# Kernel optimization log

Hardware: AMD Instinct MI355X
Metric: run time of the kernel (lower is better)

Reference implementation:

```python
import jax, jax.numpy as jnp
import numpy as np

B, S, D, H, E = 4, 1024, 1024, 16, 4
HD = D // H
FF = 4 * D
EPS = 1e-5


def _ln(x):
    # normalize only; per-expert affine applied by caller
    mu = jnp.mean(x, axis=-1, keepdims=True)
    var = jnp.mean(jnp.square(x - mu), axis=-1, keepdims=True)
    return (x - mu) * jax.lax.rsqrt(var + EPS)


def setup_inputs() -> dict:
    key = jax.random.key(0)
    ks = jax.random.split(key, 12)
    s = 0.02
    inp = {
        "x": jax.random.normal(ks[0], (B, S, D), jnp.float32),
        # attention router
        "Wr_a": jax.random.normal(ks[1], (D, E), jnp.float32) * s,
        "br_a": jnp.zeros((E,), jnp.float32),
        # per-expert attention params
        "g_a": jnp.ones((E, D), jnp.float32),
        "b_a": jnp.zeros((E, D), jnp.float32),
        "Wqkv": jax.random.normal(ks[2], (E, D, 3 * D), jnp.float32) * s,
        "bqkv": jnp.zeros((E, 3 * D), jnp.float32),
        "Wpr": jax.random.normal(ks[3], (E, D, D), jnp.float32) * s,
        "bpr": jnp.zeros((E, D), jnp.float32),
        # MLP router
        "Wr_m": jax.random.normal(ks[4], (D, E), jnp.float32) * s,
        "br_m": jnp.zeros((E,), jnp.float32),
        # per-expert MLP params
        "g_m": jnp.ones((E, D), jnp.float32),
        "b_m": jnp.zeros((E, D), jnp.float32),
        "Wfc": jax.random.normal(ks[5], (E, D, FF), jnp.float32) * s,
        "bfc": jnp.zeros((E, FF), jnp.float32),
        "Wp2": jax.random.normal(ks[6], (E, FF, D), jnp.float32) * s,
        "bp2": jnp.zeros((E, D), jnp.float32),
    }
    return inp


def _block(x, Wr_a, br_a, g_a, b_a, Wqkv, bqkv, Wpr, bpr,
           Wr_m, br_m, g_m, b_m, Wfc, bfc, Wp2, bp2):
    N = B * S
    h = x.reshape(N, D)

    # ---- MoT attention (routing_all_possible_path: dense score-weighted mix) ----
    score = jax.nn.softmax(h @ Wr_a + br_a, axis=-1)          # [N,E]
    hn = _ln(h)                                                # shared normalization
    hln = hn[None, :, :] * g_a[:, None, :] + b_a[:, None, :]  # [E,N,D]
    qkv_e = jnp.einsum('end,edf->enf', hln, Wqkv) + bqkv[:, None, :]  # [E,N,3D]
    qkv = jnp.einsum('ne,enf->nf', score, qkv_e)               # [N,3D]

    q, k, v = jnp.split(qkv.reshape(B, S, 3 * D), 3, axis=-1)
    q = q.reshape(B, S, H, HD).transpose(0, 2, 1, 3)           # [B,H,S,hd]
    k = k.reshape(B, S, H, HD).transpose(0, 2, 1, 3)
    v = v.reshape(B, S, H, HD).transpose(0, 2, 1, 3)

    aw = jnp.einsum('bhqd,bhkd->bhqk', q, k) / jnp.sqrt(jnp.float32(HD))
    causal = jnp.tril(jnp.ones((S, S), bool))
    aw = jnp.where(causal, aw, jnp.finfo(aw.dtype).min)
    p = jax.nn.softmax(aw, axis=-1)
    a = jnp.einsum('bhqk,bhkd->bhqd', p, v)                    # [B,H,S,hd]
    a = a.transpose(0, 2, 1, 3).reshape(N, D)

    attn_out = jnp.einsum('ne,nd,edf->nf', score, a, Wpr) + score @ bpr
    y = x + attn_out.reshape(B, S, D)

    # ---- MoT MLP (same dense routed-expert pattern) ----
    h2 = y.reshape(N, D)
    score2 = jax.nn.softmax(h2 @ Wr_m + br_m, axis=-1)         # [N,E]
    hn2 = _ln(h2)
    hln2 = hn2[None, :, :] * g_m[:, None, :] + b_m[:, None, :]  # [E,N,D]
    inter = jax.nn.gelu(jnp.einsum('end,edf->enf', hln2, Wfc) + bfc[:, None, :])  # [E,N,FF]
    mlp_out = jnp.einsum('ne,enf,efd->nd', score2, inter, Wp2) + score2 @ bp2
    return y + mlp_out.reshape(B, S, D)


def reference(x, Wr_a, br_a, g_a, b_a, Wqkv, bqkv, Wpr, bpr,
              Wr_m, br_m, g_m, b_m, Wfc, bfc, Wp2, bp2):
    return _block(x, Wr_a, br_a, g_a, b_a, Wqkv, bqkv, Wpr, bpr,
                  Wr_m, br_m, g_m, b_m, Wfc, bfc, Wp2, bp2)
```

## Files before the change

### kernel.cpp

```cpp
#include <hip/hip_runtime.h>
#include <hip/hip_bf16.h>

typedef __bf16 bf16x8 __attribute__((ext_vector_type(8)));
typedef float f32x4 __attribute__((ext_vector_type(4)));
typedef unsigned short u16;
typedef u16 u16x8 __attribute__((ext_vector_type(8)));
typedef u16 u16x4 __attribute__((ext_vector_type(4)));

#define B_ 4
#define S_ 1024
#define D_ 1024
#define E_ 4
#define H_ 16
#define FF_ 4096
#define N_ 4096

__device__ __forceinline__ u16 f2bf(float f) {
  __hip_bfloat16 h = __float2bfloat16(f);
  return *reinterpret_cast<u16*>(&h);
}
__device__ __forceinline__ float bf2f(u16 v) {
  return __uint_as_float(((unsigned)v) << 16);
}

#define BAR()                         \
  {                                   \
    asm volatile("" ::: "memory");    \
    __builtin_amdgcn_s_barrier();     \
    asm volatile("" ::: "memory");    \
  }

__global__ __launch_bounds__(256) void tcvt(const float* __restrict__ src,
                                            u16* __restrict__ dst, int R, int C) {
  __shared__ float t[32][33];
  int r0 = blockIdx.y * 32, c0 = blockIdx.x * 32;
  int tx = threadIdx.x, ty = threadIdx.y;
#pragma unroll
  for (int i = 0; i < 4; i++)
    t[ty + i * 8][tx] = src[(long)(r0 + ty + i * 8) * C + c0 + tx];
  __syncthreads();
#pragma unroll
  for (int i = 0; i < 4; i++)
    dst[(long)(c0 + ty + i * 8) * R + r0 + tx] = f2bf(t[tx][ty + i * 8]);
}

template <int YMODE>
__global__ __launch_bounds__(256) void ln_router_expand(
    const float* __restrict__ X, const float* __restrict__ Wr, const float* __restrict__ br,
    const float* __restrict__ g, const float* __restrict__ bb,
    float* __restrict__ score_out, u16* __restrict__ Aout,
    long stride_e, long stride_n, int scale_flag,
    const float* __restrict__ score_a, const float* __restrict__ bpr,
    const u16* __restrict__ prt, float* __restrict__ ybuf) {
  int n = blockIdx.x, t = threadIdx.x;
  int lane = t & 63, wave = t >> 6;
  int d0 = t * 4;
  const float* xr = X + (long)n * D_;
  float4 xv = *reinterpret_cast<const float4*>(&xr[d0]);
  if (YMODE) {
    float4 sa4 = reinterpret_cast<const float4*>(score_a)[n];
    float4 b0 = *reinterpret_cast<const float4*>(&bpr[d0]);
    float4 b1 = *reinterpret_cast<const float4*>(&bpr[D_ + d0]);
    float4 b2 = *reinterpret_cast<const float4*>(&bpr[2 * D_ + d0]);
    float4 b3 = *reinterpret_cast<const float4*>(&bpr[3 * D_ + d0]);
    xv.x += sa4.x * b0.x + sa4.y * b1.x + sa4.z * b2.x + sa4.w * b3.x;
    xv.y += sa4.x * b0.y + sa4.y * b1.y + sa4.z * b2.y + sa4.w * b3.y;
    xv.z += sa4.x * b0.z + sa4.y * b1.z + sa4.z * b2.z + sa4.w * b3.z;
    xv.w += sa4.x * b0.w + sa4.y * b1.w + sa4.z * b2.w + sa4.w * b3.w;
    long idx = (long)n * D_ + d0;
#pragma unroll
    for (int zz = 0; zz < 4; zz++) {
      u16x4 pv = *reinterpret_cast<const u16x4*>(&prt[(long)zz * 4194304 + idx]);
      xv.x += bf2f(pv[0]); xv.y += bf2f(pv[1]); xv.z += bf2f(pv[2]); xv.w += bf2f(pv[3]);
    }
    *reinterpret_cast<float4*>(&ybuf[idx]) = xv;
  }
  float vals[6];
  vals[0] = xv.x + xv.y + xv.z + xv.w;
  vals[1] = xv.x * xv.x + xv.y * xv.y + xv.z * xv.z + xv.w * xv.w;
  {
    float4 w0 = reinterpret_cast<const float4*>(Wr)[d0];
    float4 w1 = reinterpret_cast<const float4*>(Wr)[d0 + 1];
    float4 w2 = reinterpret_cast<const float4*>(Wr)[d0 + 2];
    float4 w3 = reinterpret_cast<const float4*>(Wr)[d0 + 3];
    vals[2] = xv.x * w0.x + xv.y * w1.x + xv.z * w2.x + xv.w * w3.x;
    vals[3] = xv.x * w0.y + xv.y * w1.y + xv.z * w2.y + xv.w * w3.y;
    vals[4] = xv.x * w0.z + xv.y * w1.z + xv.z * w2.z + xv.w * w3.z;
    vals[5] = xv.x * w0.w + xv.y * w1.w + xv.z * w2.w + xv.w * w3.w;
  }
#pragma unroll
  for (int o = 1; o < 64; o <<= 1) {
#pragma unroll
    for (int j = 0; j < 6; j++) vals[j] += __shfl_xor(vals[j], o, 64);
  }
  __shared__ float red[4][6];
  if (lane == 0) {
#pragma unroll
    for (int j = 0; j < 6; j++) red[wave][j] = vals[j];
  }
  __syncthreads();
  float tot[6];
#pragma unroll
  for (int j = 0; j < 6; j++) tot[j] = red[0][j] + red[1][j] + red[2][j] + red[3][j];
  float mean = tot[0] * (1.0f / D_);
  float var = tot[1] * (1.0f / D_) - mean * mean;
  float rstd = rsqrtf(var + 1e-5f);
  float lg0 = tot[2] + br[0], lg1 = tot[3] + br[1], lg2 = tot[4] + br[2], lg3 = tot[5] + br[3];
  float mx = fmaxf(fmaxf(lg0, lg1), fmaxf(lg2, lg3));
  float e0 = __expf(lg0 - mx), e1 = __expf(lg1 - mx), e2 = __expf(lg2 - mx), e3 = __expf(lg3 - mx);
  float inv = 1.0f / (e0 + e1 + e2 + e3);
  float sc[4] = {e0 * inv, e1 * inv, e2 * inv, e3 * inv};
  if (t == 0) {
    float4 s4 = make_float4(sc[0], sc[1], sc[2], sc[3]);
    *reinterpret_cast<float4*>(&score_out[(long)n * 4]) = s4;
  }
  float4 hn;
  hn.x = (xv.x - mean) * rstd; hn.y = (xv.y - mean) * rstd;
  hn.z = (xv.z - mean) * rstd; hn.w = (xv.w - mean) * rstd;
#pragma unroll
  for (int e = 0; e < 4; e++) {
    float4 ge = *reinterpret_cast<const float4*>(&g[e * D_ + d0]);
    float4 be = *reinterpret_cast<const float4*>(&bb[e * D_ + d0]);
    float s = scale_flag ? sc[e] : 1.0f;
    u16x4 o;
    o[0] = f2bf((hn.x * ge.x + be.x) * s);
    o[1] = f2bf((hn.y * ge.y + be.y) * s);
    o[2] = f2bf((hn.z * ge.z + be.z) * s);
    o[3] = f2bf((hn.w * ge.w + be.w) * s);
    *reinterpret_cast<u16x4*>(&Aout[(long)e * stride_e + (long)n * stride_n + d0]) = o;
  }
}

template <int MODE>
__global__ __launch_bounds__(512, 2) void g8(
    const u16* __restrict__ A, const u16* __restrict__ Bt, int K, int N, int kslice,
    const float* __restrict__ score, const float* __restrict__ bias,
    u16* __restrict__ outb, int eidx, long zstride) {
  __shared__ __align__(16) u16 lds0[65536];
  const int tid = threadIdx.x;
  const int w = tid >> 6, lane = tid & 63;
  const int l15 = lane & 15, l4 = lane >> 4;
  const int wr = w >> 2, wc = w & 3;

  const int gx = gridDim.x, gy = gridDim.y;
  const int total = gx * gy * gridDim.z;
  const int flat = blockIdx.x + gx * (blockIdx.y + gy * blockIdx.z);
  const int cpx = total >> 3;
  const int nf = (flat & 7) * cpx + (flat >> 3);
  const int bxi = nf % gx;
  const int tmp = nf / gx;
  const int byi = tmp % gy;
  const int z = tmp / gy;

  const long bm = (long)byi * 256, bn = (long)bxi * 256;
  const long k0 = (long)z * kslice;
  const int nt = kslice >> 6;

  const int cp = lane & 3;
  const int sr0 = w * 32 + (lane >> 2);
  const int sr1 = sr0 + 16;
  const int cl0 = cp ^ ((sr0 >> 1) & 3);
  const int cl1 = cp ^ ((sr1 >> 1) & 3);
  const u16* gA0 = A + (bm + sr0) * (long)K + k0 + cl0 * 8;
  const u16* gA1 = A + (bm + sr1) * (long)K + k0 + cl1 * 8;
  const u16* gB0 = Bt + (bn + sr0) * (long)K + k0 + cl0 * 8;
  const u16* gB1 = Bt + (bn + sr1) * (long)K + k0 + cl1 * 8;
  const int e0 = w * 1024;
  const int e1 = w * 1024 + 512;

  const int chA = l4 ^ ((l15 >> 1) & 3);
  const int rdA = (wr * 128 + l15) * 32 + chA * 8;
  const int rdB = (wc * 64 + l15) * 32 + chA * 8;

#define GLD(gsrc, ldsoff)                                                              \
  __builtin_amdgcn_global_load_lds(                                                    \
      (const __attribute__((address_space(1))) void*)(gsrc),                           \
      (__attribute__((address_space(3))) void*)(lds0 + (ldsoff)), 16, 0, 0)

  GLD(gA0, 0 + e0);
  GLD(gA1, 0 + e1);
  GLD(gB0, 16384 + e0);
  GLD(gB1, 16384 + e1);
  GLD(gA0 + 32, 8192 + e0);
  GLD(gA1 + 32, 8192 + e1);
  GLD(gB0 + 32, 24576 + e0);
  GLD(gB1 + 32, 24576 + e1);
  if (nt > 1) {
    GLD(gA0 + 64, 32768 + e0);
    GLD(gA1 + 64, 32768 + e1);
    GLD(gB0 + 64, 32768 + 16384 + e0);
    GLD(gB1 + 64, 32768 + 16384 + e1);
    GLD(gA0 + 96, 32768 + 8192 + e0);
    GLD(gA1 + 96, 32768 + 8192 + e1);
    GLD(gB0 + 96, 32768 + 24576 + e0);
    GLD(gB1 + 96, 32768 + 24576 + e1);
    asm volatile("s_waitcnt vmcnt(8)" ::: "memory");
  } else {
    asm volatile("s_waitcnt vmcnt(0)" ::: "memory");
  }
  BAR();

  f32x4 acc[8][4] = {};
  bf16x8 aC[8], bC[4], aN[8], bN[4];

#pragma unroll
  for (int i = 0; i < 8; i++) aC[i] = *(const bf16x8*)(lds0 + rdA + i * 512);
#pragma unroll
  for (int i = 0; i < 4; i++) bC[i] = *(const bf16x8*)(lds0 + 16384 + rdB + i * 512);

  for (int t = 0; t < nt; ++t) {
    const int base = (t & 1) * 32768;
    const int nb = base ^ 32768;
    const long ko2 = (long)(t + 2) * 64;
#pragma unroll
    for (int i = 0; i < 8; i++) aN[i] = *(const bf16x8*)(lds0 + base + 8192 + rdA + i * 512);
#pragma unroll
    for (int i = 0; i < 4; i++) bN[i] = *(const bf16x8*)(lds0 + base + 24576 + rdB + i * 512);
    if (t + 2 < nt) {
      GLD(gA0 + ko2, base + e0);
      GLD(gA1 + ko2, base + e1);
      GLD(gB0 + ko2, base + 16384 + e0);
      GLD(gB1 + ko2, base + 16384 + e1);
    }
    __builtin_amdgcn_s_setprio(1);
#pragma unroll
    for (int mi = 0; mi < 8; mi++)
#pragma unroll
      for (int ni = 0; ni < 4; ni++)
        acc[mi][ni] = __builtin_amdgcn_mfma_f32_16x16x32_bf16(aC[mi], bC[ni], acc[mi][ni], 0, 0, 0);
    __builtin_amdgcn_s_setprio(0);
    asm volatile("s_waitcnt lgkmcnt(0)" ::: "memory");
    if (t + 1 < nt) {
      if (t + 2 < nt) {
        asm volatile("s_waitcnt vmcnt(8)" ::: "memory");
      } else {
        asm volatile("s_waitcnt vmcnt(4)" ::: "memory");
      }
    }
    BAR();
    if (t + 1 < nt) {
#pragma unroll
      for (int i = 0; i < 8; i++) aC[i] = *(const bf16x8*)(lds0 + nb + rdA + i * 512);
#pragma unroll
      for (int i = 0; i < 4; i++) bC[i] = *(const bf16x8*)(lds0 + nb + 16384 + rdB + i * 512);
    }
    if (t + 2 < nt) {
      GLD(gA0 + ko2 + 32, base + 8192 + e0);
      GLD(gA1 + ko2 + 32, base + 8192 + e1);
      GLD(gB0 + ko2 + 32, base + 24576 + e0);
      GLD(gB1 + ko2 + 32, base + 24576 + e1);
    }
    __builtin_amdgcn_s_setprio(1);
#pragma unroll
    for (int mi = 0; mi < 8; mi++)
#pragma unroll
      for (int ni = 0; ni < 4; ni++)
        acc[mi][ni] = __builtin_amdgcn_mfma_f32_16x16x32_bf16(aN[mi], bN[ni], acc[mi][ni], 0, 0, 0);
    __builtin_amdgcn_s_setprio(0);
    asm volatile("s_waitcnt lgkmcnt(0)" ::: "memory");
    if (t + 1 < nt) {
      if (t + 2 < nt) {
        asm volatile("s_waitcnt vmcnt(8)" ::: "memory");
      } else {
        asm volatile("s_waitcnt vmcnt(0)" ::: "memory");
      }
    }
    BAR();
  }
#undef GLD

  const long zoff = (long)z * zstride;
#pragma unroll
  for (int ni = 0; ni < 4; ni++) {
    long col = bn + wc * 64 + ni * 16 + l15;
    float b4[4];
    float bcol = 0.0f;
    if (MODE == 0) {
#pragma unroll
      for (int e = 0; e < 4; e++) b4[e] = bias[(long)e * N + col];
    } else if (MODE == 2) {
      bcol = bias[col];
    }
#pragma unroll
    for (int mi = 0; mi < 8; mi++) {
#pragma unroll
      for (int r = 0; r < 4; r++) {
        long row = bm + wr * 128 + mi * 16 + l4 * 4 + r;
        float v = acc[mi][ni][r];
        if (MODE == 0) {
          float4 s4 = reinterpret_cast<const float4*>(score)[row];
          v += s4.x * b4[0] + s4.y * b4[1] + s4.z * b4[2] + s4.w * b4[3];
          outb[row * (long)N + col] = f2bf(v);
        } else if (MODE == 2) {
          float u = v + bcol;
          float zz = 0.7978845608f * (u + 0.044715f * u * u * u);
          float tt = __expf(2.0f * zz);
          float gel = u * (1.0f - 1.0f / (tt + 1.0f));
          outb[row * (long)N + col] = f2bf(gel * score[row * 4 + eidx]);
        } else {
          outb[zoff + row * (long)N + col] = f2bf(v);
        }
      }
    }
  }
}

__global__ __launch_bounds__(256) void attn_kernel(const u16* __restrict__ qkv,
                                                   const float* __restrict__ score_a,
                                                   u16* __restrict__ A_pr) {
  __shared__ __align__(16) u16 Kt[32 * 64];
  __shared__ __align__(16) u16 VT[64 * 32];
  __shared__ __align__(16) u16 Pl[4][16 * 32];
  int tid = threadIdx.x, wave = tid >> 6, lane = tid & 63;
  int l15 = lane & 15, l4 = lane >> 4;
  int qblk = blockIdx.x, bh = blockIdx.y;
  int b = bh >> 4, h = bh & 15;
  int q0 = qblk * 64 + wave * 16;
  const long LD = 3072;

  bf16x8 qf[2];
  {
    const u16* qp = qkv + (long)(b * 1024 + q0 + l15) * LD + h * 64 + l4 * 8;
    qf[0] = *(const bf16x8*)qp;
    qf[1] = *(const bf16x8*)(qp + 32);
  }
  f32x4 acc[4] = {};
  float m_run = -1e30f, l_run = 0.0f;
  int kv_end = qblk * 64 + 64;

  for (int kv0 = 0; kv0 < kv_end; kv0 += 32) {
    {
      int r = tid >> 3, c = (tid & 7) * 8;
      const u16* kp = qkv + (long)(b * 1024 + kv0 + r) * LD + 1024 + h * 64 + c;
      *(u16x8*)&Kt[r * 64 + c] = *(const u16x8*)kp;
      u16x8 vv = *(const u16x8*)(kp + 1024);
#pragma unroll
      for (int j = 0; j < 8; j++) VT[(c + j) * 32 + r] = vv[j];
    }
    __syncthreads();
    if (kv0 < q0 + 16) {
      float p[8];
      float pmax = -1e30f;
      int qg = q0 + l15;
#pragma unroll
      for (int ks = 0; ks < 2; ks++) {
        f32x4 st = {};
#pragma unroll
        for (int kc = 0; kc < 2; kc++) {
          bf16x8 kf = *(const bf16x8*)&Kt[(ks * 16 + l15) * 64 + kc * 32 + l4 * 8];
          st = __builtin_amdgcn_mfma_f32_16x16x32_bf16(kf, qf[kc], st, 0, 0, 0);
        }
#pragma unroll
        for (int r = 0; r < 4; r++) {
          int kvg = kv0 + ks * 16 + l4 * 4 + r;
          float v = st[r] * 0.125f;
          if (kvg > qg) v = -1e30f;
          p[ks * 4 + r] = v;
          pmax = fmaxf(pmax, v);
        }
      }
      pmax = fmaxf(pmax, __shfl_xor(pmax, 16, 64));
      pmax = fmaxf(pmax, __shfl_xor(pmax, 32, 64));
      float m_new = fmaxf(m_run, pmax);
      float alpha = __expf(m_run - m_new);
      float rsum = 0.f;
#pragma unroll
      for (int i = 0; i < 8; i++) {
        p[i] = __expf(p[i] - m_new);
        rsum += p[i];
      }
      rsum += __shfl_xor(rsum, 16, 64);
      rsum += __shfl_xor(rsum, 32, 64);
      l_run = l_run * alpha + rsum;
      m_run = m_new;
      float af4[4];
#pragma unroll
      for (int r = 0; r < 4; r++) af4[r] = __shfl(alpha, l4 * 4 + r, 64);
#pragma unroll
      for (int i = 0; i < 4; i++) {
#pragma unroll
        for (int r = 0; r < 4; r++) acc[i][r] *= af4[r];
      }
      u16* pw = &Pl[wave][0];
#pragma unroll
      for (int i = 0; i < 8; i++) {
        int ks = i >> 2, r = i & 3;
        pw[l15 * 32 + ks * 16 + l4 * 4 + r] = f2bf(p[i]);
      }
      bf16x8 pa = *(const bf16x8*)&pw[l15 * 32 + l4 * 8];
#pragma unroll
      for (int i = 0; i < 4; i++) {
        bf16x8 vf = *(const bf16x8*)&VT[(i * 16 + l15) * 32 + l4 * 8];
        acc[i] = __builtin_amdgcn_mfma_f32_16x16x32_bf16(pa, vf, acc[i], 0, 0, 0);
      }
    }
    __syncthreads();
  }

  float linv[4];
#pragma unroll
  for (int r = 0; r < 4; r++) {
    float lv = __shfl(l_run, l4 * 4 + r, 64);
    linv[r] = 1.0f / lv;
  }
#pragma unroll
  for (int r = 0; r < 4; r++) {
    int q = l4 * 4 + r;
    long nrow = (long)b * 1024 + q0 + q;
    float4 s4 = reinterpret_cast<const float4*>(score_a)[nrow];
    float se[4] = {s4.x, s4.y, s4.z, s4.w};
#pragma unroll
    for (int i = 0; i < 4; i++) {
      float v = acc[i][r] * linv[r];
      int d = h * 64 + i * 16 + l15;
#pragma unroll
      for (int e = 0; e < 4; e++) A_pr[nrow * 4096 + e * 1024 + d] = f2bf(se[e] * v);
    }
  }
}

template <int FIRST>
__global__ __launch_bounds__(256) void accum_out(const float* __restrict__ ybuf,
                                                 const float* __restrict__ score_m,
                                                 const float* __restrict__ bp2,
                                                 const u16* __restrict__ p2t,
                                                 float* __restrict__ out) {
  int n = blockIdx.x, t = threadIdx.x;
  int d0 = t * 4;
  long idx = (long)n * D_ + d0;
  float4 v;
  if (FIRST) {
    float4 s4 = reinterpret_cast<const float4*>(score_m)[n];
    float4 b0 = *reinterpret_cast<const float4*>(&bp2[d0]);
    float4 b1 = *reinterpret_cast<const float4*>(&bp2[D_ + d0]);
    float4 b2 = *reinterpret_cast<const float4*>(&bp2[2 * D_ + d0]);
    float4 b3 = *reinterpret_cast<const float4*>(&bp2[3 * D_ + d0]);
    v = *reinterpret_cast<const float4*>(&ybuf[idx]);
    v.x += s4.x * b0.x + s4.y * b1.x + s4.z * b2.x + s4.w * b3.x;
    v.y += s4.x * b0.y + s4.y * b1.y + s4.z * b2.y + s4.w * b3.y;
    v.z += s4.x * b0.z + s4.y * b1.z + s4.z * b2.z + s4.w * b3.z;
    v.w += s4.x * b0.w + s4.y * b1.w + s4.z * b2.w + s4.w * b3.w;
  } else {
    v = *reinterpret_cast<const float4*>(&out[idx]);
  }
#pragma unroll
  for (int zz = 0; zz < 4; zz++) {
    u16x4 pv = *reinterpret_cast<const u16x4*>(&p2t[(long)zz * 4194304 + idx]);
    v.x += bf2f(pv[0]); v.y += bf2f(pv[1]); v.z += bf2f(pv[2]); v.w += bf2f(pv[3]);
  }
  *reinterpret_cast<float4*>(&out[idx]) = v;
}

extern "C" void kernel_launch(void* const* d_in, const int* in_sizes, int n_in, void* d_out,
                              int out_size, void* d_ws, size_t ws_size, hipStream_t stream) {
  (void)in_sizes; (void)n_in; (void)out_size; (void)ws_size;
  const float* x    = (const float*)d_in[0];
  const float* Wr_a = (const float*)d_in[1];
  const float* br_a = (const float*)d_in[2];
  const float* g_a  = (const float*)d_in[3];
  const float* b_a  = (const float*)d_in[4];
  const float* Wqkv = (const float*)d_in[5];
  const float* bqkv = (const float*)d_in[6];
  const float* Wpr  = (const float*)d_in[7];
  const float* bpr  = (const float*)d_in[8];
  const float* Wr_m = (const float*)d_in[9];
  const float* br_m = (const float*)d_in[10];
  const float* g_m  = (const float*)d_in[11];
  const float* b_m  = (const float*)d_in[12];
  const float* Wfc  = (const float*)d_in[13];
  const float* bfc  = (const float*)d_in[14];
  const float* Wp2  = (const float*)d_in[15];
  const float* bp2  = (const float*)d_in[16];
  float* out = (float*)d_out;

  char* ws = (char*)d_ws;
  const size_t oW = 0;
  const size_t oA = 25165824;
  const size_t oQ = oA + 33554432;
  const size_t oP = oQ + 33554432;
  const size_t oY = oP + 33554432;
  const size_t oS = oY + 16777216;
  u16* wt_qkv  = (u16*)(ws + oW);
  u16* wt_pr   = (u16*)(ws + oW);
  u16* wt_fce  = (u16*)(ws + oW);
  u16* wt_p2e  = (u16*)(ws + oW + (size_t)8 * 1024 * 1024);
  u16* A_a     = (u16*)(ws + oA);
  u16* prt     = (u16*)(ws + oA);
  u16* A_fc    = (u16*)(ws + oA);
  u16* qkvb    = (u16*)(ws + oQ);
  u16* p2t     = (u16*)(ws + oQ);
  u16* A_pr    = (u16*)(ws + oP);
  u16* inter   = (u16*)(ws + oP);
  float* ybuf  = (float*)(ws + oY);
  float* score_a = (float*)(ws + oS);
  float* score_m = (float*)(ws + oS + 65536);

  dim3 tb(32, 8);
  tcvt<<<dim3(3072 / 32, 4096 / 32), tb, 0, stream>>>(Wqkv, wt_qkv, 4096, 3072);
  ln_router_expand<0><<<N_, 256, 0, stream>>>(x, Wr_a, br_a, g_a, b_a, score_a, A_a,
                                              (long)1024, (long)4096, 1,
                                              nullptr, nullptr, nullptr, nullptr);
  g8<0><<<dim3(3072 / 256, 4096 / 256, 1), 512, 0, stream>>>(
      A_a, wt_qkv, 4096, 3072, 4096, score_a, bqkv, qkvb, 0, 0L);
  attn_kernel<<<dim3(S_ / 64, B_ * H_), 256, 0, stream>>>(qkvb, score_a, A_pr);
  tcvt<<<dim3(1024 / 32, 4096 / 32), tb, 0, stream>>>(Wpr, wt_pr, 4096, 1024);
  g8<4><<<dim3(1024 / 256, 4096 / 256, 4), 512, 0, stream>>>(
      A_pr, wt_pr, 4096, 1024, 1024, nullptr, nullptr, prt, 0, (long)4096 * 1024);

  ln_router_expand<1><<<N_, 256, 0, stream>>>(x, Wr_m, br_m, g_m, b_m,
                                              score_m, A_fc, (long)N_ * 1024, (long)1024, 0,
                                              score_a, bpr, prt, ybuf);
  for (int e = 0; e < 4; e++) {
    tcvt<<<dim3(4096 / 32, 1024 / 32), tb, 0, stream>>>(
        Wfc + (size_t)e * 1024 * 4096, wt_fce, 1024, 4096);
    g8<2><<<dim3(4096 / 256, 4096 / 256, 1), 512, 0, stream>>>(
        A_fc + (size_t)e * N_ * 1024, wt_fce, 1024, 4096, 1024, score_m,
        bfc + e * 4096, inter, e, 0L);
    tcvt<<<dim3(1024 / 32, 4096 / 32), tb, 0, stream>>>(
        Wp2 + (size_t)e * 4096 * 1024, wt_p2e, 4096, 1024);
    g8<4><<<dim3(1024 / 256, 4096 / 256, 4), 512, 0, stream>>>(
        inter, wt_p2e, 4096, 1024, 1024, nullptr, nullptr, p2t, 0, (long)4096 * 1024);
    if (e == 0) {
      accum_out<1><<<N_, 256, 0, stream>>>(ybuf, score_m, bp2, p2t, out);
    } else {
      accum_out<0><<<N_, 256, 0, stream>>>(nullptr, nullptr, nullptr, p2t, out);
    }
  }
}
```

Measured before the change: 789.4 us.

## Batch expert projection by per-expert weights and apply scores after attention

The attention output is no longer expanded into four score-scaled copies (an N×4D matrix). The projection GEMM now runs as a batched z-over-experts product of the shared attention output with each expert's Wpr, and the router scores are applied when the four partial outputs are summed in the residual kernel. This cuts the A-matrix write and read traffic and the K length of that GEMM by a factor of four. Weight conversions for Wfc and Wp2 are batched into single launches over the experts, which needs a larger workspace layout. Scheduling barriers are added before the MFMA blocks in the GEMM.

```diff
diff --git a/kernel.cpp b/kernel.cpp
--- a/kernel.cpp
+++ b/kernel.cpp
@@ -33,6 +33,8 @@
 __global__ __launch_bounds__(256) void tcvt(const float* __restrict__ src,
                                             u16* __restrict__ dst, int R, int C) {
   __shared__ float t[32][33];
+  long base = (long)blockIdx.z * R * C;
+  src += base; dst += base;
   int r0 = blockIdx.y * 32, c0 = blockIdx.x * 32;
   int tx = threadIdx.x, ty = threadIdx.y;
 #pragma unroll
@@ -59,6 +61,7 @@
   float4 xv = *reinterpret_cast<const float4*>(&xr[d0]);
   if (YMODE) {
     float4 sa4 = reinterpret_cast<const float4*>(score_a)[n];
+    float sw[4] = {sa4.x, sa4.y, sa4.z, sa4.w};
     float4 b0 = *reinterpret_cast<const float4*>(&bpr[d0]);
     float4 b1 = *reinterpret_cast<const float4*>(&bpr[D_ + d0]);
     float4 b2 = *reinterpret_cast<const float4*>(&bpr[2 * D_ + d0]);
@@ -71,7 +74,8 @@
 #pragma unroll
     for (int zz = 0; zz < 4; zz++) {
       u16x4 pv = *reinterpret_cast<const u16x4*>(&prt[(long)zz * 4194304 + idx]);
-      xv.x += bf2f(pv[0]); xv.y += bf2f(pv[1]); xv.z += bf2f(pv[2]); xv.w += bf2f(pv[3]);
+      xv.x += sw[zz] * bf2f(pv[0]); xv.y += sw[zz] * bf2f(pv[1]);
+      xv.z += sw[zz] * bf2f(pv[2]); xv.w += sw[zz] * bf2f(pv[3]);
     }
     *reinterpret_cast<float4*>(&ybuf[idx]) = xv;
   }
@@ -135,7 +139,7 @@
 __global__ __launch_bounds__(512, 2) void g8(
     const u16* __restrict__ A, const u16* __restrict__ Bt, int K, int N, int kslice,
     const float* __restrict__ score, const float* __restrict__ bias,
-    u16* __restrict__ outb, int eidx, long zstride) {
+    u16* __restrict__ outb, int eidx, long zstride, long bz) {
   __shared__ __align__(16) u16 lds0[65536];
   const int tid = threadIdx.x;
   const int w = tid >> 6, lane = tid & 63;
@@ -153,7 +157,8 @@
   const int z = tmp / gy;
 
   const long bm = (long)byi * 256, bn = (long)bxi * 256;
-  const long k0 = (long)z * kslice;
+  const long k0 = bz ? 0L : (long)z * kslice;
+  const u16* Btz = bz ? (Bt + (long)z * bz) : Bt;
   const int nt = kslice >> 6;
 
   const int cp = lane & 3;
@@ -163,8 +168,8 @@
   const int cl1 = cp ^ ((sr1 >> 1) & 3);
   const u16* gA0 = A + (bm + sr0) * (long)K + k0 + cl0 * 8;
   const u16* gA1 = A + (bm + sr1) * (long)K + k0 + cl1 * 8;
-  const u16* gB0 = Bt + (bn + sr0) * (long)K + k0 + cl0 * 8;
-  const u16* gB1 = Bt + (bn + sr1) * (long)K + k0 + cl1 * 8;
+  const u16* gB0 = Btz + (bn + sr0) * (long)K + k0 + cl0 * 8;
+  const u16* gB1 = Btz + (bn + sr1) * (long)K + k0 + cl1 * 8;
   const int e0 = w * 1024;
   const int e1 = w * 1024 + 512;
 
@@ -222,6 +227,7 @@
       GLD(gB0 + ko2, base + 16384 + e0);
       GLD(gB1 + ko2, base + 16384 + e1);
     }
+    __builtin_amdgcn_sched_barrier(0);
     __builtin_amdgcn_s_setprio(1);
 #pragma unroll
     for (int mi = 0; mi < 8; mi++)
@@ -250,6 +256,7 @@
       GLD(gB0 + ko2 + 32, base + 24576 + e0);
       GLD(gB1 + ko2 + 32, base + 24576 + e1);
     }
+    __builtin_amdgcn_sched_barrier(0);
     __builtin_amdgcn_s_setprio(1);
 #pragma unroll
     for (int mi = 0; mi < 8; mi++)
@@ -306,8 +313,7 @@
 }
 
 __global__ __launch_bounds__(256) void attn_kernel(const u16* __restrict__ qkv,
-                                                   const float* __restrict__ score_a,
-                                                   u16* __restrict__ A_pr) {
+                                                   u16* __restrict__ aout) {
   __shared__ __align__(16) u16 Kt[32 * 64];
   __shared__ __align__(16) u16 VT[64 * 32];
   __shared__ __align__(16) u16 Pl[4][16 * 32];
@@ -407,14 +413,10 @@
   for (int r = 0; r < 4; r++) {
     int q = l4 * 4 + r;
     long nrow = (long)b * 1024 + q0 + q;
-    float4 s4 = reinterpret_cast<const float4*>(score_a)[nrow];
-    float se[4] = {s4.x, s4.y, s4.z, s4.w};
 #pragma unroll
     for (int i = 0; i < 4; i++) {
-      float v = acc[i][r] * linv[r];
       int d = h * 64 + i * 16 + l15;
-#pragma unroll
-      for (int e = 0; e < 4; e++) A_pr[nrow * 4096 + e * 1024 + d] = f2bf(se[e] * v);
+      aout[nrow * 1024 + d] = f2bf(acc[i][r] * linv[r]);
     }
   }
 }
@@ -474,52 +476,53 @@
   float* out = (float*)d_out;
 
   char* ws = (char*)d_ws;
-  const size_t oW = 0;
-  const size_t oA = 25165824;
-  const size_t oQ = oA + 33554432;
-  const size_t oP = oQ + 33554432;
-  const size_t oY = oP + 33554432;
-  const size_t oS = oY + 16777216;
-  u16* wt_qkv  = (u16*)(ws + oW);
-  u16* wt_pr   = (u16*)(ws + oW);
-  u16* wt_fce  = (u16*)(ws + oW);
-  u16* wt_p2e  = (u16*)(ws + oW + (size_t)8 * 1024 * 1024);
-  u16* A_a     = (u16*)(ws + oA);
-  u16* prt     = (u16*)(ws + oA);
-  u16* A_fc    = (u16*)(ws + oA);
-  u16* qkvb    = (u16*)(ws + oQ);
-  u16* p2t     = (u16*)(ws + oQ);
-  u16* A_pr    = (u16*)(ws + oP);
-  u16* inter   = (u16*)(ws + oP);
-  float* ybuf  = (float*)(ws + oY);
-  float* score_a = (float*)(ws + oS);
-  float* score_m = (float*)(ws + oS + 65536);
+  const size_t R1 = 0;
+  const size_t R2 = 33554432;
+  const size_t R3 = 67108864;
+  const size_t R4 = 100663296;
+  const size_t R5 = 134217728;
+  const size_t R6 = 167772160;
+  const size_t R7 = 184549376;
+  u16* wt_qkv  = (u16*)(ws + R1);
+  u16* wt_pr   = (u16*)(ws + R1);
+  u16* wt_fc   = (u16*)(ws + R1);
+  u16* wt_p2   = (u16*)(ws + R2);
+  u16* A_a     = (u16*)(ws + R2);
+  u16* qkvb    = (u16*)(ws + R3);
+  u16* A_fc    = (u16*)(ws + R3);
+  u16* abuf    = (u16*)(ws + R4);
+  u16* inter   = (u16*)(ws + R4);
+  u16* prt     = (u16*)(ws + R5);
+  u16* p2t     = (u16*)(ws + R5);
+  float* ybuf  = (float*)(ws + R6);
+  float* score_a = (float*)(ws + R7);
+  float* score_m = (float*)(ws + R7 + 65536);
 
   dim3 tb(32, 8);
-  tcvt<<<dim3(3072 / 32, 4096 / 32), tb, 0, stream>>>(Wqkv, wt_qkv, 4096, 3072);
+  tcvt<<<dim3(3072 / 32, 4096 / 32, 1), tb, 0, stream>>>(Wqkv, wt_qkv, 4096, 3072);
   ln_router_expand<0><<<N_, 256, 0, stream>>>(x, Wr_a, br_a, g_a, b_a, score_a, A_a,
                                               (long)1024, (long)4096, 1,
                                               nullptr, nullptr, nullptr, nullptr);
   g8<0><<<dim3(3072 / 256, 4096 / 256, 1), 512, 0, stream>>>(
-      A_a, wt_qkv, 4096, 3072, 4096, score_a, bqkv, qkvb, 0, 0L);
-  attn_kernel<<<dim3(S_ / 64, B_ * H_), 256, 0, stream>>>(qkvb, score_a, A_pr);
-  tcvt<<<dim3(1024 / 32, 4096 / 32), tb, 0, stream>>>(Wpr, wt_pr, 4096, 1024);
+      A_a, wt_qkv, 4096, 3072, 4096, score_a, bqkv, qkvb, 0, 0L, 0L);
+  attn_kernel<<<dim3(S_ / 64, B_ * H_), 256, 0, stream>>>(qkvb, abuf);
+  tcvt<<<dim3(1024 / 32, 1024 / 32, 4), tb, 0, stream>>>(Wpr, wt_pr, 1024, 1024);
   g8<4><<<dim3(1024 / 256, 4096 / 256, 4), 512, 0, stream>>>(
-      A_pr, wt_pr, 4096, 1024, 1024, nullptr, nullptr, prt, 0, (long)4096 * 1024);
-
+      abuf, wt_pr, 1024, 1024, 1024, nullptr, nullptr, prt, 0,
+      (long)4096 * 1024, (long)1024 * 1024);
+
+  tcvt<<<dim3(4096 / 32, 1024 / 32, 4), tb, 0, stream>>>(Wfc, wt_fc, 1024, 4096);
+  tcvt<<<dim3(1024 / 32, 4096 / 32, 4), tb, 0, stream>>>(Wp2, wt_p2, 4096, 1024);
   ln_router_expand<1><<<N_, 256, 0, stream>>>(x, Wr_m, br_m, g_m, b_m,
                                               score_m, A_fc, (long)N_ * 1024, (long)1024, 0,
                                               score_a, bpr, prt, ybuf);
   for (int e = 0; e < 4; e++) {
-    tcvt<<<dim3(4096 / 32, 1024 / 32), tb, 0, stream>>>(
-        Wfc + (size_t)e * 1024 * 4096, wt_fce, 1024, 4096);
     g8<2><<<dim3(4096 / 256, 4096 / 256, 1), 512, 0, stream>>>(
-        A_fc + (size_t)e * N_ * 1024, wt_fce, 1024, 4096, 1024, score_m,
-        bfc + e * 4096, inter, e, 0L);
-    tcvt<<<dim3(1024 / 32, 4096 / 32), tb, 0, stream>>>(
-        Wp2 + (size_t)e * 4096 * 1024, wt_p2e, 4096, 1024);
+        A_fc + (size_t)e * N_ * 1024, wt_fc + (size_t)e * 4096 * 1024, 1024, 4096, 1024,
+        score_m, bfc + e * 4096, inter, e, 0L, 0L);
     g8<4><<<dim3(1024 / 256, 4096 / 256, 4), 512, 0, stream>>>(
-        inter, wt_p2e, 4096, 1024, 1024, nullptr, nullptr, p2t, 0, (long)4096 * 1024);
+        inter, wt_p2 + (size_t)e * 1024 * 4096, 4096, 1024, 1024, nullptr, nullptr,
+        p2t, 0, (long)4096 * 1024, 0L);
     if (e == 0) {
       accum_out<1><<<N_, 256, 0, stream>>>(ybuf, score_m, bp2, p2t, out);
     } else {
```

Result: no change. 791.8 us (+0.3%).
